# Performance work log

Hardware: AMD Instinct MI355X
Metric: run time of the kernel (lower is better)

The kernel has to match this reference:

```python
import jax, jax.numpy as jnp
import numpy as np

N = 50000
E = 600000
IN_DIM = 256
OUT_DIM = 128
SCALE = 1.8
K = 2
ALPHA = 0.15
EPS = 1e-12  # matches F.normalize eps


def setup_inputs() -> dict:
    key = jax.random.key(0)
    k1, k2, k3, k4 = jax.random.split(key, 4)
    x = jax.random.normal(k1, (N, IN_DIM), dtype=jnp.float32)
    edge_index = jax.random.randint(k2, (2, E), 0, N, dtype=jnp.int64)
    # nn.Linear params (Kaiming-uniform-ish init scale)
    lim = 1.0 / np.sqrt(IN_DIM)
    W = jax.random.uniform(k3, (OUT_DIM, IN_DIM), dtype=jnp.float32, minval=-lim, maxval=lim)
    b = jax.random.uniform(k4, (OUT_DIM,), dtype=jnp.float32, minval=-lim, maxval=lim)
    return {"x": x, "edge_index": edge_index, "W": W, "b": b}


def _gcn_norm(edge_index, num_nodes):
    # add self loops, symmetric normalization D^-1/2 A D^-1/2
    loops = jnp.arange(num_nodes, dtype=edge_index.dtype)
    row = jnp.concatenate([edge_index[0], loops])  # source
    col = jnp.concatenate([edge_index[1], loops])  # target
    deg = jax.ops.segment_sum(jnp.ones_like(col, dtype=jnp.float32), col,
                              num_segments=num_nodes)
    dinv = jnp.where(deg > 0, jax.lax.rsqrt(deg), 0.0)
    w = dinv[row] * dinv[col]
    return row, col, w


def reference(x, edge_index, W, b):
    # linear
    h = x @ W.T + b  # [N, OUT_DIM]
    # L2 normalize over feature dim, then scale
    nrm = jnp.sqrt(jnp.sum(h * h, axis=1, keepdims=True))
    h = h / jnp.maximum(nrm, EPS) * SCALE
    # APPNP propagation (eval mode: edge dropout disabled)
    row, col, w = _gcn_norm(edge_index, N)
    z = h
    for _ in range(K):
        msg = w[:, None] * z[row]  # gather + weight, [E+N, OUT_DIM]
        agg = jax.ops.segment_sum(msg, col, num_segments=N)
        z = (1.0 - ALPHA) * agg + ALPHA * h
    return z
```

## Files before the change

kernel.cpp:

```cpp
#include <hip/hip_runtime.h>
#include <hip/hip_bf16.h>

#define NNODES 50000
#define IN_DIM 256
#define OUT_DIM 128
#define SCALE 1.8f
#define ALPHA 0.15f
#define NB_SCAN 196

typedef unsigned short ushort_t;
typedef __attribute__((ext_vector_type(8))) _Float16 f16x8;
typedef __attribute__((ext_vector_type(4))) float f32x4;


__device__ __forceinline__ unsigned short f2bf_rne(float f) {
    unsigned int u = __float_as_uint(f);
    unsigned int r = u + 0x7fffu + ((u >> 16) & 1u);
    return (unsigned short)(r >> 16);
}

__device__ __forceinline__ float2 bf2_to_f2(unsigned int p) {
    float2 f;
    f.x = __uint_as_float(p << 16);
    f.y = __uint_as_float(p & 0xffff0000u);
    return f;
}

__device__ __forceinline__ unsigned int f2_to_bf2(float x, float y) {
    return (unsigned int)f2bf_rne(x) | ((unsigned int)f2bf_rne(y) << 16);
}

__device__ __forceinline__ unsigned short f2h(float f) {
    _Float16 h = (_Float16)f;
    return *(unsigned short*)&h;
}


__global__ void deg_scatter_kernel(const int* __restrict__ col, int* __restrict__ cnt, int E) {
    int e = blockIdx.x * blockDim.x + threadIdx.x;
    if (e < E) atomicAdd(&cnt[col[e]], 1);
}


__global__ void wcvt_kernel(const float* __restrict__ W, ushort_t* __restrict__ Whf) {
    int i = blockIdx.x * blockDim.x + threadIdx.x;
    if (i < OUT_DIM * IN_DIM) Whf[i] = f2h(W[i]);
}


__global__ void scan_pass1(const int* __restrict__ cnt, int* __restrict__ part) {
    __shared__ int sd[256];
    int t = threadIdx.x;
    int i = blockIdx.x * 256 + t;
    sd[t] = (i < NNODES) ? cnt[i] : 0;
    __syncthreads();
    for (int s = 128; s > 0; s >>= 1) {
        if (t < s) sd[t] += sd[t + s];
        __syncthreads();
    }
    if (t == 0) part[blockIdx.x] = sd[0];
}

__global__ void scan_pass2(int* __restrict__ part) {
    __shared__ int s[256];
    int t = threadIdx.x;
    int v = (t < NB_SCAN) ? part[t] : 0;
    s[t] = v;
    __syncthreads();
    for (int o = 1; o < 256; o <<= 1) {
        int u = (t >= o) ? s[t - o] : 0;
        __syncthreads();
        s[t] += u;
        __syncthreads();
    }
    if (t < NB_SCAN) part[t] = (t == 0) ? 0 : s[t - 1];
}

__global__ void scan_pass3(const int* __restrict__ cnt, const int* __restrict__ part,
                           int* __restrict__ off, int* __restrict__ cur,
                           float* __restrict__ dinv, float* __restrict__ q,
                           float2* __restrict__ gr, int E) {
    __shared__ int s[256];
    int t = threadIdx.x;
    int i = blockIdx.x * 256 + t;
    int v = (i < NNODES) ? cnt[i] : 0;
    s[t] = v;
    __syncthreads();
    for (int o = 1; o < 256; o <<= 1) {
        int u = (t >= o) ? s[t - o] : 0;
        __syncthreads();
        s[t] += u;
        __syncthreads();
    }
    int excl = part[blockIdx.x] + ((t == 0) ? 0 : s[t - 1]);
    if (i < NNODES) {
        off[i] = excl;
        cur[i] = excl;
        float deg = (float)(v + 1);
        float d = rsqrtf(deg);
        dinv[i] = d;
        q[i] = (1.0f - ALPHA) * d * d;
        gr[i] = make_float2((1.0f - ALPHA) * d, ALPHA * sqrtf(deg));
    }
    if (i == NNODES - 1) off[NNODES] = E;
}

__global__ void csr_fill_kernel(const int* __restrict__ row, const int* __restrict__ col,
                                int* __restrict__ cur, int* __restrict__ csr_row, int E) {
    int e = blockIdx.x * blockDim.x + threadIdx.x;
    if (e < E) {
        int c = col[e];
        int p = atomicAdd(&cur[c], 1);
        csr_row[p] = row[e];
    }
}


#define XPAD 264

__global__ void __launch_bounds__(256, 4) gemm_norm_kernel(
        const float* __restrict__ x, const ushort_t* __restrict__ Whf,
        const float* __restrict__ b, const float* __restrict__ dinv,
        ushort_t* __restrict__ s0b) {
    __shared__ __align__(16) ushort_t xh[64][XPAD];

    const int t = threadIdx.x;
    const int wv = t >> 6;
    const int lane = t & 63;
    const int q = lane >> 4;
    const int c = lane & 15;
    const int rowBase = blockIdx.x * 64;

    f16x8 wf[2][8];
    float bias[2];
    #pragma unroll
    for (int j = 0; j < 2; ++j) {
        const size_t base = (size_t)((2 * wv + j) * 16 + c) * IN_DIM + q * 8;
        #pragma unroll
        for (int kt = 0; kt < 8; ++kt)
            wf[j][kt] = *(const f16x8*)(Whf + base + kt * 32);
        bias[j] = b[(2 * wv + j) * 16 + c];
    }

    #pragma unroll
    for (int it = 0; it < 16; ++it) {
        int s = it * 256 + t;
        int r = s >> 6;
        int ks = (s & 63) * 4;
        int grow = rowBase + r;
        float4 v = make_float4(0.f, 0.f, 0.f, 0.f);
        if (grow < NNODES) v = *(const float4*)(x + (size_t)grow * IN_DIM + ks);
        uint2 p;
        p.x = (unsigned int)f2h(v.x) | ((unsigned int)f2h(v.y) << 16);
        p.y = (unsigned int)f2h(v.z) | ((unsigned int)f2h(v.w) << 16);
        *(uint2*)&xh[r][ks] = p;
    }
    __syncthreads();

    f32x4 acc[4][2];
    #pragma unroll
    for (int m = 0; m < 4; ++m)
        #pragma unroll
        for (int j = 0; j < 2; ++j) {
            acc[m][j][0] = bias[j]; acc[m][j][1] = bias[j];
            acc[m][j][2] = bias[j]; acc[m][j][3] = bias[j];
        }

    #pragma unroll
    for (int kt = 0; kt < 8; ++kt) {
        const int kb = kt * 32 + q * 8;
        #pragma unroll
        for (int m = 0; m < 4; ++m) {
            f16x8 a = *(const f16x8*)&xh[m * 16 + c][kb];
            #pragma unroll
            for (int j = 0; j < 2; ++j)
                acc[m][j] = __builtin_amdgcn_mfma_f32_16x16x32_f16(a, wf[j][kt], acc[m][j], 0, 0, 0);
        }
    }

    float psum[4][4];
    #pragma unroll
    for (int m = 0; m < 4; ++m)
        #pragma unroll
        for (int r = 0; r < 4; ++r)
            psum[m][r] = acc[m][0][r] * acc[m][0][r] + acc[m][1][r] * acc[m][1][r];
    #pragma unroll
    for (int mask = 1; mask < 16; mask <<= 1)
        #pragma unroll
        for (int m = 0; m < 4; ++m)
            #pragma unroll
            for (int r = 0; r < 4; ++r)
                psum[m][r] += __shfl_xor(psum[m][r], mask);

    __syncthreads();
    float* red = (float*)&xh[0][0];
    float* scl = red + 64 * 8;
    if (c == 0) {
        #pragma unroll
        for (int m = 0; m < 4; ++m)
            #pragma unroll
            for (int r = 0; r < 4; ++r)
                red[(m * 16 + q * 4 + r) * 8 + wv] = psum[m][r];
    }
    __syncthreads();
    if (t < 64) {
        float s = red[t * 8 + 0] + red[t * 8 + 1] + red[t * 8 + 2] + red[t * 8 + 3];
        scl[t] = dinv[rowBase + t] * SCALE / fmaxf(sqrtf(s), 1e-12f);
    }
    __syncthreads();

    #pragma unroll
    for (int m = 0; m < 4; ++m) {
        #pragma unroll
        for (int r = 0; r < 4; ++r) {
            int lrow = m * 16 + q * 4 + r;
            int grow = rowBase + lrow;
            if (grow < NNODES) {
                float sc = scl[lrow];
                #pragma unroll
                for (int j = 0; j < 2; ++j) {
                    float o = acc[m][j][r] * sc;
                    s0b[(size_t)grow * OUT_DIM + (2 * wv + j) * 16 + c] = f2bf_rne(o);
                }
            }
        }
    }
}


template <int FINAL>
__global__ void __launch_bounds__(256) gather_kernel(
        const int* __restrict__ off, const int* __restrict__ csr_row,
        const float* __restrict__ q, const float2* __restrict__ gr,
        const unsigned int* __restrict__ sin, const unsigned int* __restrict__ s0,
        unsigned int* __restrict__ sout_b, float* __restrict__ out_f) {
    const int wv = threadIdx.x >> 6;
    const int lane = threadIdx.x & 63;
    const int c = blockIdx.x * 4 + wv;
    const int s = off[c];
    const int e = off[c + 1];

    float2 acc;
    float2 zc0;
    {
        float2 zc = bf2_to_f2(sin[(size_t)c * 64 + lane]);
        acc = zc;
        zc0 = FINAL ? bf2_to_f2(s0[(size_t)c * 64 + lane]) : zc;
    }

    for (int base = s; base < e; base += 64) {
        int n = e - base;
        if (n > 64) n = 64;
        int idx = 0;
        if (lane < n) idx = csr_row[base + lane];
        int j = 0;
        for (; j + 4 <= n; j += 4) {
            int r0 = __shfl(idx, j + 0), r1 = __shfl(idx, j + 1);
            int r2 = __shfl(idx, j + 2), r3 = __shfl(idx, j + 3);
            unsigned int p0 = sin[(size_t)r0 * 64 + lane];
            unsigned int p1 = sin[(size_t)r1 * 64 + lane];
            unsigned int p2 = sin[(size_t)r2 * 64 + lane];
            unsigned int p3 = sin[(size_t)r3 * 64 + lane];
            float2 v0 = bf2_to_f2(p0), v1 = bf2_to_f2(p1);
            float2 v2 = bf2_to_f2(p2), v3 = bf2_to_f2(p3);
            acc.x += v0.x + v1.x + v2.x + v3.x;
            acc.y += v0.y + v1.y + v2.y + v3.y;
        }
        for (; j < n; ++j) {
            int r = __shfl(idx, j);
            float2 v = bf2_to_f2(sin[(size_t)r * 64 + lane]);
            acc.x += v.x;
            acc.y += v.y;
        }
    }

    if (FINAL) {
        float2 g = gr[c];
        float ox = g.x * acc.x + g.y * zc0.x;
        float oy = g.x * acc.y + g.y * zc0.y;
        ((float2*)out_f)[(size_t)c * 64 + lane] = make_float2(ox, oy);
    } else {
        float qc = q[c];
        float ox = qc * acc.x + ALPHA * zc0.x;
        float oy = qc * acc.y + ALPHA * zc0.y;
        sout_b[(size_t)c * 64 + lane] = f2_to_bf2(ox, oy);
    }
}

extern "C" void kernel_launch(void* const* d_in, const int* in_sizes, int n_in,
                              void* d_out, int out_size, void* d_ws, size_t ws_size,
                              hipStream_t stream) {
    const float* x  = (const float*)d_in[0];
    const int*   ei = (const int*)d_in[1];
    const float* W  = (const float*)d_in[2];
    const float* b  = (const float*)d_in[3];
    float* out = (float*)d_out;

    int E = in_sizes[1] / 2;
    const int* row = ei;
    const int* col = ei + E;

    float*  dinv = (float*)d_ws;
    float*  q    = dinv + 50048;
    float2* gr   = (float2*)(q + 50048);
    unsigned int* s0b = (unsigned int*)(gr + 50048);
    unsigned int* s1b = s0b + (size_t)NNODES * 64;
    int*   cnt   = (int*)(s1b + (size_t)NNODES * 64);
    int*   off   = cnt + 50048;
    int*   cur   = off + 50112;
    int*   part  = cur + 50048;
    int*   csr_row = part + 256;
    ushort_t* Whf  = (ushort_t*)(csr_row + ((E + 63) & ~63));

    hipMemsetAsync(cnt, 0, NNODES * sizeof(int), stream);
    deg_scatter_kernel<<<(E + 255) / 256, 256, 0, stream>>>(col, cnt, E);
    wcvt_kernel<<<(OUT_DIM * IN_DIM + 255) / 256, 256, 0, stream>>>(W, Whf);

    scan_pass1<<<NB_SCAN, 256, 0, stream>>>(cnt, part);
    scan_pass2<<<1, 256, 0, stream>>>(part);
    scan_pass3<<<NB_SCAN, 256, 0, stream>>>(cnt, part, off, cur, dinv, q, gr, E);
    csr_fill_kernel<<<(E + 255) / 256, 256, 0, stream>>>(row, col, cur, csr_row, E);

    gemm_norm_kernel<<<(NNODES + 63) / 64, 256, 0, stream>>>(x, Whf, b, dinv, (ushort_t*)s0b);

    gather_kernel<0><<<NNODES / 4, 256, 0, stream>>>(off, csr_row, q, gr, s0b, s0b, s1b, nullptr);
    gather_kernel<1><<<NNODES / 4, 256, 0, stream>>>(off, csr_row, q, gr, s1b, s0b, nullptr, out);
}
```

Measured before the change: 237.1 us.

## Split node features into column-chunk planes and gather chunks in separate grid slices

The bf16 feature matrix is stored as four column-chunk planes of 32 features each, written that way by the GEMM epilogue. Each gather block handles one chunk, selected by blockIdx.y. Each wavefront processes four neighbors at a time, one per 16-lane quarter, and combines the partial sums with cross-lane shuffles. The aim is to shrink the per-chunk working set so each plane fits better in cache, and to increase parallelism. The cost is re-reading the CSR indices once per chunk, issuing narrower 64-byte loads, and leaving lanes idle in the epilogue.

```diff
diff --git a/kernel.cpp b/kernel.cpp
--- a/kernel.cpp
+++ b/kernel.cpp
@@ -220,13 +220,16 @@
                 #pragma unroll
                 for (int j = 0; j < 2; ++j) {
                     float o = acc[m][j][r] * sc;
-                    s0b[(size_t)grow * OUT_DIM + (2 * wv + j) * 16 + c] = f2bf_rne(o);
+                    s0b[((size_t)wv * NNODES + grow) * 32 + j * 16 + c] = f2bf_rne(o);
                 }
             }
         }
     }
 }
 
+
+#define CHUNK_U32 16
+#define NCHUNK 4
 
 template <int FINAL>
 __global__ void __launch_bounds__(256) gather_kernel(
@@ -236,54 +239,58 @@
         unsigned int* __restrict__ sout_b, float* __restrict__ out_f) {
     const int wv = threadIdx.x >> 6;
     const int lane = threadIdx.x & 63;
+    const int qd = lane >> 4;
+    const int d = lane & 15;
+    const int chunk = blockIdx.y;
     const int c = blockIdx.x * 4 + wv;
+
+    const unsigned int* __restrict__ sin_c = sin + (size_t)chunk * (NNODES * CHUNK_U32);
+
     const int s = off[c];
     const int e = off[c + 1];
 
-    float2 acc;
-    float2 zc0;
-    {
-        float2 zc = bf2_to_f2(sin[(size_t)c * 64 + lane]);
-        acc = zc;
-        zc0 = FINAL ? bf2_to_f2(s0[(size_t)c * 64 + lane]) : zc;
-    }
+    float2 acc = make_float2(0.f, 0.f);
 
     for (int base = s; base < e; base += 64) {
         int n = e - base;
         if (n > 64) n = 64;
         int idx = 0;
         if (lane < n) idx = csr_row[base + lane];
-        int j = 0;
-        for (; j + 4 <= n; j += 4) {
-            int r0 = __shfl(idx, j + 0), r1 = __shfl(idx, j + 1);
-            int r2 = __shfl(idx, j + 2), r3 = __shfl(idx, j + 3);
-            unsigned int p0 = sin[(size_t)r0 * 64 + lane];
-            unsigned int p1 = sin[(size_t)r1 * 64 + lane];
-            unsigned int p2 = sin[(size_t)r2 * 64 + lane];
-            unsigned int p3 = sin[(size_t)r3 * 64 + lane];
-            float2 v0 = bf2_to_f2(p0), v1 = bf2_to_f2(p1);
-            float2 v2 = bf2_to_f2(p2), v3 = bf2_to_f2(p3);
-            acc.x += v0.x + v1.x + v2.x + v3.x;
-            acc.y += v0.y + v1.y + v2.y + v3.y;
-        }
-        for (; j < n; ++j) {
-            int r = __shfl(idx, j);
-            float2 v = bf2_to_f2(sin[(size_t)r * 64 + lane]);
-            acc.x += v.x;
-            acc.y += v.y;
-        }
-    }
-
-    if (FINAL) {
-        float2 g = gr[c];
-        float ox = g.x * acc.x + g.y * zc0.x;
-        float oy = g.x * acc.y + g.y * zc0.y;
-        ((float2*)out_f)[(size_t)c * 64 + lane] = make_float2(ox, oy);
-    } else {
-        float qc = q[c];
-        float ox = qc * acc.x + ALPHA * zc0.x;
-        float oy = qc * acc.y + ALPHA * zc0.y;
-        sout_b[(size_t)c * 64 + lane] = f2_to_bf2(ox, oy);
+        for (int j = 0; j < n; j += 4) {
+            int r = __shfl(idx, j + qd);
+            if (j + qd < n) {
+                float2 v = bf2_to_f2(sin_c[(size_t)r * CHUNK_U32 + d]);
+                acc.x += v.x;
+                acc.y += v.y;
+            }
+        }
+    }
+
+    acc.x += __shfl_xor(acc.x, 16);
+    acc.y += __shfl_xor(acc.y, 16);
+    acc.x += __shfl_xor(acc.x, 32);
+    acc.y += __shfl_xor(acc.y, 32);
+
+    if (qd == 0) {
+        float2 zc = bf2_to_f2(sin_c[(size_t)c * CHUNK_U32 + d]);
+        acc.x += zc.x;
+        acc.y += zc.y;
+        if (FINAL) {
+            const unsigned int* __restrict__ s0_c =
+                s0 + (size_t)chunk * (NNODES * CHUNK_U32);
+            float2 z0 = bf2_to_f2(s0_c[(size_t)c * CHUNK_U32 + d]);
+            float2 g = gr[c];
+            float ox = g.x * acc.x + g.y * z0.x;
+            float oy = g.x * acc.y + g.y * z0.y;
+            ((float2*)out_f)[(size_t)c * 64 + chunk * 16 + d] = make_float2(ox, oy);
+        } else {
+            unsigned int* __restrict__ sout_c =
+                sout_b + (size_t)chunk * (NNODES * CHUNK_U32);
+            float qc = q[c];
+            float ox = qc * acc.x + ALPHA * zc.x;
+            float oy = qc * acc.y + ALPHA * zc.y;
+            sout_c[(size_t)c * CHUNK_U32 + d] = f2_to_bf2(ox, oy);
+        }
     }
 }
 
@@ -323,6 +330,7 @@
 
     gemm_norm_kernel<<<(NNODES + 63) / 64, 256, 0, stream>>>(x, Whf, b, dinv, (ushort_t*)s0b);
 
-    gather_kernel<0><<<NNODES / 4, 256, 0, stream>>>(off, csr_row, q, gr, s0b, s0b, s1b, nullptr);
-    gather_kernel<1><<<NNODES / 4, 256, 0, stream>>>(off, csr_row, q, gr, s1b, s0b, nullptr, out);
-}
+    dim3 ggrid(NNODES / 4, NCHUNK);
+    gather_kernel<0><<<ggrid, 256, 0, stream>>>(off, csr_row, q, gr, s0b, s0b, s1b, nullptr);
+    gather_kernel<1><<<ggrid, 256, 0, stream>>>(off, csr_row, q, gr, s1b, s0b, nullptr, out);
+}
```

Result: slower. 323.2 us (+36.3%).

## Gather four neighbor rows per wave with 16-byte loads and cross-quarter reduction

Applied to the files above, without the earlier changes.

The CSR gather kernel now splits each 64-lane wave into four 16-lane groups. Each group reads a whole 256-byte bf16 row with uint4 loads, so four neighbors are processed per load step instead of one row per wave with 4-byte loads. Partial sums are combined with xor-shuffles, and one quarter applies the self term and writes the output with vectorized stores. This cuts load instructions and raises memory-level parallelism, but it adds shuffle reductions and leaves three quarters of the lanes idle in the epilogue.

```diff
diff --git a/kernel.cpp b/kernel.cpp
--- a/kernel.cpp
+++ b/kernel.cpp
@@ -228,6 +228,15 @@
 }
 
 
+__device__ __forceinline__ void acc_row4(float2* a, uint4 v) {
+    float2 f0 = bf2_to_f2(v.x), f1 = bf2_to_f2(v.y);
+    float2 f2 = bf2_to_f2(v.z), f3 = bf2_to_f2(v.w);
+    a[0].x += f0.x; a[0].y += f0.y;
+    a[1].x += f1.x; a[1].y += f1.y;
+    a[2].x += f2.x; a[2].y += f2.y;
+    a[3].x += f3.x; a[3].y += f3.y;
+}
+
 template <int FINAL>
 __global__ void __launch_bounds__(256) gather_kernel(
         const int* __restrict__ off, const int* __restrict__ csr_row,
@@ -236,17 +245,16 @@
         unsigned int* __restrict__ sout_b, float* __restrict__ out_f) {
     const int wv = threadIdx.x >> 6;
     const int lane = threadIdx.x & 63;
+    const int qd = lane >> 4;
+    const int d16 = lane & 15;
     const int c = blockIdx.x * 4 + wv;
+
     const int s = off[c];
     const int e = off[c + 1];
 
-    float2 acc;
-    float2 zc0;
-    {
-        float2 zc = bf2_to_f2(sin[(size_t)c * 64 + lane]);
-        acc = zc;
-        zc0 = FINAL ? bf2_to_f2(s0[(size_t)c * 64 + lane]) : zc;
-    }
+    float2 a[4];
+    #pragma unroll
+    for (int k = 0; k < 4; ++k) a[k] = make_float2(0.f, 0.f);
 
     for (int base = s; base < e; base += 64) {
         int n = e - base;
@@ -254,36 +262,69 @@
         int idx = 0;
         if (lane < n) idx = csr_row[base + lane];
         int j = 0;
-        for (; j + 4 <= n; j += 4) {
-            int r0 = __shfl(idx, j + 0), r1 = __shfl(idx, j + 1);
-            int r2 = __shfl(idx, j + 2), r3 = __shfl(idx, j + 3);
-            unsigned int p0 = sin[(size_t)r0 * 64 + lane];
-            unsigned int p1 = sin[(size_t)r1 * 64 + lane];
-            unsigned int p2 = sin[(size_t)r2 * 64 + lane];
-            unsigned int p3 = sin[(size_t)r3 * 64 + lane];
-            float2 v0 = bf2_to_f2(p0), v1 = bf2_to_f2(p1);
-            float2 v2 = bf2_to_f2(p2), v3 = bf2_to_f2(p3);
-            acc.x += v0.x + v1.x + v2.x + v3.x;
-            acc.y += v0.y + v1.y + v2.y + v3.y;
-        }
-        for (; j < n; ++j) {
-            int r = __shfl(idx, j);
-            float2 v = bf2_to_f2(sin[(size_t)r * 64 + lane]);
-            acc.x += v.x;
-            acc.y += v.y;
-        }
-    }
-
-    if (FINAL) {
-        float2 g = gr[c];
-        float ox = g.x * acc.x + g.y * zc0.x;
-        float oy = g.x * acc.y + g.y * zc0.y;
-        ((float2*)out_f)[(size_t)c * 64 + lane] = make_float2(ox, oy);
-    } else {
-        float qc = q[c];
-        float ox = qc * acc.x + ALPHA * zc0.x;
-        float oy = qc * acc.y + ALPHA * zc0.y;
-        sout_b[(size_t)c * 64 + lane] = f2_to_bf2(ox, oy);
+        for (; j + 8 <= n; j += 8) {
+            int r0 = __shfl(idx, j + qd);
+            int r1 = __shfl(idx, j + 4 + qd);
+            uint4 v0 = *(const uint4*)(sin + (size_t)r0 * 64 + d16 * 4);
+            uint4 v1 = *(const uint4*)(sin + (size_t)r1 * 64 + d16 * 4);
+            acc_row4(a, v0);
+            acc_row4(a, v1);
+        }
+        for (; j < n; j += 4) {
+            int jj = j + qd;
+            int r0 = __shfl(idx, (jj < n) ? jj : (n - 1));
+            if (jj < n) {
+                uint4 v0 = *(const uint4*)(sin + (size_t)r0 * 64 + d16 * 4);
+                acc_row4(a, v0);
+            }
+        }
+    }
+
+    #pragma unroll
+    for (int k = 0; k < 4; ++k) {
+        a[k].x += __shfl_xor(a[k].x, 16);
+        a[k].y += __shfl_xor(a[k].y, 16);
+        a[k].x += __shfl_xor(a[k].x, 32);
+        a[k].y += __shfl_xor(a[k].y, 32);
+    }
+
+    if (qd == 0) {
+        uint4 zc4 = *(const uint4*)(sin + (size_t)c * 64 + d16 * 4);
+        float2 zc[4];
+        zc[0] = bf2_to_f2(zc4.x); zc[1] = bf2_to_f2(zc4.y);
+        zc[2] = bf2_to_f2(zc4.z); zc[3] = bf2_to_f2(zc4.w);
+        #pragma unroll
+        for (int k = 0; k < 4; ++k) {
+            a[k].x += zc[k].x;
+            a[k].y += zc[k].y;
+        }
+        if (FINAL) {
+            uint4 z04 = *(const uint4*)(s0 + (size_t)c * 64 + d16 * 4);
+            float2 z0[4];
+            z0[0] = bf2_to_f2(z04.x); z0[1] = bf2_to_f2(z04.y);
+            z0[2] = bf2_to_f2(z04.z); z0[3] = bf2_to_f2(z04.w);
+            float2 g = gr[c];
+            float4 o0, o1;
+            o0.x = g.x * a[0].x + g.y * z0[0].x;
+            o0.y = g.x * a[0].y + g.y * z0[0].y;
+            o0.z = g.x * a[1].x + g.y * z0[1].x;
+            o0.w = g.x * a[1].y + g.y * z0[1].y;
+            o1.x = g.x * a[2].x + g.y * z0[2].x;
+            o1.y = g.x * a[2].y + g.y * z0[2].y;
+            o1.z = g.x * a[3].x + g.y * z0[3].x;
+            o1.w = g.x * a[3].y + g.y * z0[3].y;
+            float* p = out_f + (size_t)c * 128 + d16 * 8;
+            *(float4*)(p) = o0;
+            *(float4*)(p + 4) = o1;
+        } else {
+            float qc = q[c];
+            uint4 w;
+            w.x = f2_to_bf2(qc * a[0].x + ALPHA * zc[0].x, qc * a[0].y + ALPHA * zc[0].y);
+            w.y = f2_to_bf2(qc * a[1].x + ALPHA * zc[1].x, qc * a[1].y + ALPHA * zc[1].y);
+            w.z = f2_to_bf2(qc * a[2].x + ALPHA * zc[2].x, qc * a[2].y + ALPHA * zc[2].y);
+            w.w = f2_to_bf2(qc * a[3].x + ALPHA * zc[3].x, qc * a[3].y + ALPHA * zc[3].y);
+            *(uint4*)(sout_b + (size_t)c * 64 + d16 * 4) = w;
+        }
     }
 }
 
```

Result: faster. 232.3 us (-2.0%).
